# Kernel tuning notes

Measured on AMD Instinct MI355X. Metric: run time of the kernel, lower is better.

Reference implementation:

```python
import jax, jax.numpy as jnp
import numpy as np

B, T, N, D_OBJ = 8, 32, 10, 2048
N_VERB, N_OBJCLS = 157, 353
D_EMB, D_VERB = 512, 2048


def setup_inputs() -> dict:
    key = jax.random.key(0)
    k1, k2, k3, k4, k5 = jax.random.split(key, 5)
    objects_features = jax.random.normal(k1, (B, T, N, D_OBJ), dtype=jnp.float32)
    fm_context = jax.random.normal(k2, (B, T, D_VERB), dtype=jnp.float32)
    obj_id = jax.random.randint(k3, (B, T, N, N_OBJCLS), 0, 2, dtype=jnp.int32)
    W = jax.random.normal(k4, (D_OBJ, D_EMB), dtype=jnp.float32) * 0.02
    b = jnp.zeros((D_EMB,), dtype=jnp.float32)
    A_o2v = jnp.full((N_VERB, N_OBJCLS), 1.0 / N_VERB, dtype=jnp.float32)
    return {"objects_features": objects_features, "fm_context": fm_context,
            "obj_id": obj_id, "W": W, "b": b, "A_o2v": A_o2v}


def reference(objects_features, fm_context, obj_id, W, b, A_o2v):
    D = obj_id.shape[-1]
    # one-hot cleanup: all-zero row -> class 0; multi-hot row -> last nonzero class
    row_sum = obj_id.sum(-1)                                  # (B,T,N)
    last_nz = (D - 1) - jnp.argmax(jnp.flip(obj_id, -1), -1)  # last nonzero index
    cls = jnp.where(row_sum == 0, 0, last_nz)                 # (B,T,N)

    obj_embedded = objects_features @ W + b                   # (B,T,N,D_emb)

    # subA[b,t,n,v] = A_o2v[v, cls[b,t,n]]
    subA = A_o2v.T[cls]                                       # (B,T,N,V)

    afforded = jnp.einsum('btnv,btnd->btvd', subA, obj_embedded)  # (B,T,V,D_emb)

    V = A_o2v.shape[0]
    ctx = jnp.broadcast_to(fm_context[:, :, None, :],
                           (afforded.shape[0], afforded.shape[1], V, fm_context.shape[-1]))
    vo_actions = jnp.concatenate([afforded, ctx], axis=-1)    # (B,T,V,D_emb+D_verb)
    return vo_actions.mean(axis=1)                            # (B,V,D_emb+D_verb)
```

## Files before the change

kernel.cpp:

```cpp
#include <hip/hip_runtime.h>


typedef __attribute__((ext_vector_type(8))) short short8;
typedef __attribute__((ext_vector_type(8))) unsigned short us8;
typedef __attribute__((ext_vector_type(4))) unsigned short us4;
typedef __attribute__((ext_vector_type(4))) float f32x4;

#define OFF_CTX  0
#define OFF_SAT  65536
#define OFF_WT   1048576
#define OFF_PART 3145728

static __device__ inline unsigned short f2bf(float x) {
    unsigned int u = __builtin_bit_cast(unsigned int, x);
    u += 0x7fffu + ((u >> 16) & 1u);
    return (unsigned short)(u >> 16);
}
static __device__ inline void gl16(const void* g, void* l) {
    __builtin_amdgcn_global_load_lds(
        (__attribute__((address_space(1))) void*)(g),
        (__attribute__((address_space(3))) void*)(l), 16, 0, 0);
}

__global__ __launch_bounds__(256) void k_prep(
    const float* __restrict__ W, const float* __restrict__ fm,
    const int* __restrict__ obj, const float* __restrict__ A,
    unsigned short* __restrict__ Wt, float* __restrict__ ctx,
    unsigned short* __restrict__ sAT)
{
    __shared__ float t[32][33];
    __shared__ int lcls[64];
    int bx = blockIdx.x, tid = threadIdx.x;

    if (bx < 1024) {
        int r0 = (bx >> 4) * 32, c0 = (bx & 15) * 32;
        int rr = tid >> 3, cc = (tid & 7) * 4;
        float4 v = *(const float4*)&W[(size_t)(r0 + rr) * 512 + c0 + cc];
        t[rr][cc] = v.x; t[rr][cc+1] = v.y; t[rr][cc+2] = v.z; t[rr][cc+3] = v.w;
        __syncthreads();
        us4 o = { f2bf(t[cc][rr]), f2bf(t[cc+1][rr]), f2bf(t[cc+2][rr]), f2bf(t[cc+3][rr]) };
        *(us4*)&Wt[(size_t)(c0 + rr) * 2048 + r0 + cc] = o;
    } else if (bx < 1088) {
        int id = (bx - 1024) * 256 + tid;
        int b = id >> 11, d = id & 2047;
        const float* p = fm + (size_t)b * 32 * 2048 + d;
        float s = 0.f;
        #pragma unroll
        for (int tt = 0; tt < 32; tt++) s += p[(size_t)tt * 2048];
        ctx[id] = s * (1.0f / 32.0f);
    } else {
        int blk = bx - 1088;
        int b = blk / 5, i0 = (blk % 5) * 64;
        int w = tid >> 6, lane = tid & 63;
        for (int rr = 0; rr < 16; rr++) {
            int il = w * 16 + rr;
            const int* p = obj + ((size_t)b * 320 + i0 + il) * 353;
            int last = -1;
            #pragma unroll
            for (int base = 0; base < 384; base += 64) {
                int idx = base + lane;
                int v = (idx < 353) ? p[idx] : 0;
                unsigned long long m = __ballot(v != 0);
                if (m) last = base + 63 - __clzll(m);
            }
            if (lane == 0) lcls[il] = (last < 0) ? 0 : last;
        }
        __syncthreads();
        #pragma unroll
        for (int q = 0; q < 6; q++) {
            int u = q * 256 + tid;
            int v = u >> 3, i8 = u & 7;
            us8 o = {};
            if (v < 157) {
                #pragma unroll
                for (int j = 0; j < 8; j++)
                    o[j] = f2bf(A[v * 353 + lcls[i8 * 8 + j]] * (1.0f / 32.0f));
            }
            *(us8*)&sAT[((size_t)b * 192 + v) * 320 + i0 + i8 * 8] = o;
        }
    }
}

__global__ __launch_bounds__(256) void k_gemmE(
    const float* __restrict__ feat, const unsigned short* __restrict__ Wt,
    float* __restrict__ part)
{
    int bx = blockIdx.x;
    int ks = bx & 3, nt = (bx >> 2) & 3, mt = bx >> 4;
    int m0 = mt * 64, n0 = nt * 128, k0 = ks * 512;
    int b = m0 / 320, i0 = m0 % 320;

    __shared__ __align__(16) unsigned short la[2][64 * 64];
    __shared__ __align__(16) unsigned short lb[2][128 * 64];

    int tid = threadIdx.x, lane = tid & 63, w = tid >> 6;
    int wm = (w >> 1) * 32, wn = (w & 1) * 64;
    int fr = lane & 15, fk = lane >> 4;

    int ar = tid >> 2, acol = (tid & 3) * 16;
    const float* gA = feat + (size_t)(m0 + ar) * 2048 + k0 + acol;
    int asl0 = ((tid & 3) * 2 + 0) ^ (ar & 7);
    int asl1 = ((tid & 3) * 2 + 1) ^ (ar & 7);

    const unsigned short* gB[4];
    #pragma unroll
    for (int c = 0; c < 4; c++) {
        int s = c * 256 + tid, er = s >> 3, ch = s & 7;
        gB[c] = Wt + (size_t)(n0 + er) * 2048 + k0 + ((ch ^ (er & 7)) << 3);
    }

    f32x4 acc[2][4] = {};
    f32x4 a4[4];

    auto loadA = [&](int kk) {
        #pragma unroll
        for (int j = 0; j < 4; j++) a4[j] = *(const f32x4*)(gA + kk + j * 4);
    };
    auto stageB = [&](int buf, int kk) {
        #pragma unroll
        for (int c = 0; c < 4; c++)
            gl16(gB[c] + kk, &lb[buf][(c * 256 + tid) * 8]);
    };
    auto writeA = [&](int buf) {
        us8 o0, o1;
        #pragma unroll
        for (int j = 0; j < 4; j++) { o0[j] = f2bf(a4[0][j]); o0[j+4] = f2bf(a4[1][j]); }
        #pragma unroll
        for (int j = 0; j < 4; j++) { o1[j] = f2bf(a4[2][j]); o1[j+4] = f2bf(a4[3][j]); }
        *(us8*)&la[buf][ar * 64 + (asl0 << 3)] = o0;
        *(us8*)&la[buf][ar * 64 + (asl1 << 3)] = o1;
    };
    auto compute = [&](int buf) {
        #pragma unroll
        for (int k2 = 0; k2 < 2; k2++) {
            short8 af[2], bf[4];
            #pragma unroll
            for (int mi = 0; mi < 2; mi++) {
                int r = wm + mi * 16 + fr;
                af[mi] = *(const short8*)&la[buf][r * 64 + (((k2 * 4 + fk) ^ (r & 7)) << 3)];
            }
            #pragma unroll
            for (int ni = 0; ni < 4; ni++) {
                int r = wn + ni * 16 + fr;
                bf[ni] = *(const short8*)&lb[buf][r * 64 + (((k2 * 4 + fk) ^ (r & 7)) << 3)];
            }
            #pragma unroll
            for (int mi = 0; mi < 2; mi++)
                #pragma unroll
                for (int ni = 0; ni < 4; ni++)
                    acc[mi][ni] = __builtin_amdgcn_mfma_f32_16x16x32_bf16(
                        af[mi], bf[ni], acc[mi][ni], 0, 0, 0);
        }
    };

    loadA(0); stageB(0, 0); writeA(0);
    __syncthreads();
    int cur = 0;
    #pragma unroll 1
    for (int t = 0; t < 8; t++) {
        if (t < 7) { loadA((t + 1) * 64); stageB(cur ^ 1, (t + 1) * 64); }
        compute(cur);
        if (t < 7) writeA(cur ^ 1);
        __syncthreads();
        cur ^= 1;
    }

    #pragma unroll
    for (int mi = 0; mi < 2; mi++) {
        int i = i0 + wm + mi * 16 + fk * 4;
        #pragma unroll
        for (int ni = 0; ni < 4; ni++) {
            int e = n0 + wn + ni * 16 + fr;
            *(f32x4*)&part[((size_t)(b * 512 + e) * 4 + ks) * 320 + i] = acc[mi][ni];
        }
    }
}

__global__ __launch_bounds__(256) void k_out(
    const unsigned short* __restrict__ sAT, const float* __restrict__ part,
    const float* __restrict__ bias, const float* __restrict__ ctx,
    float* __restrict__ out)
{
    if (blockIdx.x >= 96) {
        int id = (blockIdx.x - 96) * 256 + threadIdx.x;
        int q = id & 511, bv = id >> 9, b = bv / 157;
        float4 v = *(const float4*)&ctx[((size_t)b << 11) + q * 4];
        *(float4*)&out[(size_t)bv * 2560 + 512 + q * 4] = v;
        return;
    }
    int bx = blockIdx.x;
    int b = bx / 12, r = bx % 12;
    int v0 = (r >> 2) * 64, e0 = (r & 3) * 128;

    __shared__ __align__(16) unsigned short la[2][64 * 32];
    __shared__ __align__(16) unsigned short lb[2][128 * 32];

    int tid = threadIdx.x, lane = tid & 63, w = tid >> 6;
    int wm = (w >> 1) * 32, wn = (w & 1) * 64;
    int fr = lane & 15, fk = lane >> 4;

    int aer = tid >> 2, ach = tid & 3;
    const unsigned short* gA = sAT + ((size_t)b * 192 + v0 + aer) * 320
                                   + ((ach ^ (aer & 3)) << 3);
    const float* pb = part + (size_t)b * 512 * 4 * 320;

    f32x4 acc[2][4] = {};
    f32x4 s0, s1, s2, s3;
    float be0, be1, be2, be3;

    auto loadB = [&](int kk) {
        f32x4* sp[4] = { &s0, &s1, &s2, &s3 };
        float* bp[4] = { &be0, &be1, &be2, &be3 };
        #pragma unroll
        for (int q = 0; q < 4; q++) {
            int u = q * 256 + tid, e = u >> 3, i4 = u & 7;
            const float* base = pb + (size_t)(e0 + e) * 4 * 320 + kk + i4 * 4;
            f32x4 s = *(const f32x4*)(base);
            s += *(const f32x4*)(base + 320);
            s += *(const f32x4*)(base + 640);
            s += *(const f32x4*)(base + 960);
            *sp[q] = s;
            *bp[q] = bias[e0 + e];
        }
    };
    auto writeB = [&](int buf) {
        f32x4 sv[4] = { s0, s1, s2, s3 };
        float bv[4] = { be0, be1, be2, be3 };
        #pragma unroll
        for (int q = 0; q < 4; q++) {
            int u = q * 256 + tid, e = u >> 3, i4 = u & 7;
            f32x4 s = sv[q];
            float be = bv[q];
            us4 o = { f2bf(s[0] + be), f2bf(s[1] + be), f2bf(s[2] + be), f2bf(s[3] + be) };
            *(us4*)&lb[buf][e * 32 + ((((i4 >> 1) ^ (e & 3)) << 3) + (i4 & 1) * 4)] = o;
        }
    };
    auto compute = [&](int buf) {
        short8 af[2], bf[4];
        #pragma unroll
        for (int mi = 0; mi < 2; mi++) {
            int rr = wm + mi * 16 + fr;
            af[mi] = *(const short8*)&la[buf][rr * 32 + ((fk ^ (rr & 3)) << 3)];
        }
        #pragma unroll
        for (int ni = 0; ni < 4; ni++) {
            int rr = wn + ni * 16 + fr;
            bf[ni] = *(const short8*)&lb[buf][rr * 32 + ((fk ^ (rr & 3)) << 3)];
        }
        #pragma unroll
        for (int mi = 0; mi < 2; mi++)
            #pragma unroll
            for (int ni = 0; ni < 4; ni++)
                acc[mi][ni] = __builtin_amdgcn_mfma_f32_16x16x32_bf16(
                    af[mi], bf[ni], acc[mi][ni], 0, 0, 0);
    };

    gl16(gA, &la[0][tid * 8]);
    loadB(0); writeB(0);
    __syncthreads();
    int cur = 0;
    #pragma unroll 1
    for (int t = 0; t < 10; t++) {
        if (t < 9) { gl16(gA + (t + 1) * 32, &la[cur ^ 1][tid * 8]); loadB((t + 1) * 32); }
        compute(cur);
        if (t < 9) writeB(cur ^ 1);
        __syncthreads();
        cur ^= 1;
    }

    #pragma unroll
    for (int mi = 0; mi < 2; mi++) {
        int vb = v0 + wm + mi * 16 + fk * 4;
        #pragma unroll
        for (int ni = 0; ni < 4; ni++) {
            int e = e0 + wn + ni * 16 + fr;
            #pragma unroll
            for (int rr = 0; rr < 4; rr++) {
                int v = vb + rr;
                if (v < 157)
                    out[((size_t)b * 157 + v) * 2560 + e] = acc[mi][ni][rr];
            }
        }
    }
}

extern "C" void kernel_launch(void* const* d_in, const int* in_sizes, int n_in,
                              void* d_out, int out_size, void* d_ws, size_t ws_size,
                              hipStream_t stream)
{
    const float* feat = (const float*)d_in[0];
    const float* fm   = (const float*)d_in[1];
    const int*   obj  = (const int*)d_in[2];
    const float* W    = (const float*)d_in[3];
    const float* bias = (const float*)d_in[4];
    const float* A    = (const float*)d_in[5];
    float* out = (float*)d_out;

    char* ws = (char*)d_ws;
    float*          ctx  = (float*)(ws + OFF_CTX);
    unsigned short* sAT  = (unsigned short*)(ws + OFF_SAT);
    unsigned short* Wt   = (unsigned short*)(ws + OFF_WT);
    float*          part = (float*)(ws + OFF_PART);

    k_prep <<<1128, 256, 0, stream>>>(W, fm, obj, A, Wt, ctx, sAT);
    k_gemmE<<<640, 256, 0, stream>>>(feat, Wt, part);
    k_out  <<<2608, 256, 0, stream>>>(sAT, part, bias, ctx, out);
}
```

Measured before the change: 128.9 us.

## Pre-convert features to bf16 and split class extraction into own kernel

Adds a pass in k_prep that converts the fp32 object features to bf16 in workspace, so the GEMM can stage both A and B tiles straight into LDS with global_load_lds instead of loading fp32 into registers and converting. The one-hot class decoding moves into a separate k_cls kernel with one wavefront per row, rather than serial loops inside the sAT blocks. The aim is to cut register pressure and latency in the GEMM main loop. In exchange the features are read in fp32 and written and reread in bf16 (about 10 MB extra traffic), and there is one more kernel launch.

```diff
diff --git a/kernel.cpp b/kernel.cpp
--- a/kernel.cpp
+++ b/kernel.cpp
@@ -9,7 +9,9 @@
 #define OFF_CTX  0
 #define OFF_SAT  65536
 #define OFF_WT   1048576
-#define OFF_PART 3145728
+#define OFF_FB   3145728
+#define OFF_PART 13631488
+#define OFF_CLS  39845888
 
 static __device__ inline unsigned short f2bf(float x) {
     unsigned int u = __builtin_bit_cast(unsigned int, x);
@@ -22,26 +24,55 @@
         (__attribute__((address_space(3))) void*)(l), 16, 0, 0);
 }
 
+__global__ void k_cls(const int* __restrict__ obj_id, int* __restrict__ cls)
+{
+    int row  = blockIdx.x * 4 + (threadIdx.x >> 6);
+    int lane = threadIdx.x & 63;
+    if (row >= 2560) return;
+    const int* p = obj_id + (size_t)row * 353;
+    int last = -1;
+    #pragma unroll
+    for (int base = 0; base < 384; base += 64) {
+        int idx = base + lane;
+        int v = (idx < 353) ? p[idx] : 0;
+        unsigned long long m = __ballot(v != 0);
+        if (m) last = base + 63 - __clzll(m);
+    }
+    if (lane == 0) cls[row] = (last < 0) ? 0 : last;
+}
+
 __global__ __launch_bounds__(256) void k_prep(
     const float* __restrict__ W, const float* __restrict__ fm,
-    const int* __restrict__ obj, const float* __restrict__ A,
+    const float* __restrict__ feat, const int* __restrict__ cls,
+    const float* __restrict__ A,
     unsigned short* __restrict__ Wt, float* __restrict__ ctx,
-    unsigned short* __restrict__ sAT)
+    unsigned short* __restrict__ featb, unsigned short* __restrict__ sAT)
 {
     __shared__ float t[32][33];
     __shared__ int lcls[64];
     int bx = blockIdx.x, tid = threadIdx.x;
 
-    if (bx < 1024) {
-        int r0 = (bx >> 4) * 32, c0 = (bx & 15) * 32;
+    if (bx < 1280) {
+        size_t id = (size_t)bx * 256 + tid;
+        const float* p = feat + id * 16;
+        us8 o0, o1;
+        #pragma unroll
+        for (int j = 0; j < 8; j++) o0[j] = f2bf(p[j]);
+        #pragma unroll
+        for (int j = 0; j < 8; j++) o1[j] = f2bf(p[8 + j]);
+        *(us8*)&featb[id * 16] = o0;
+        *(us8*)&featb[id * 16 + 8] = o1;
+    } else if (bx < 2304) {
+        int b2 = bx - 1280;
+        int r0 = (b2 >> 4) * 32, c0 = (b2 & 15) * 32;
         int rr = tid >> 3, cc = (tid & 7) * 4;
         float4 v = *(const float4*)&W[(size_t)(r0 + rr) * 512 + c0 + cc];
         t[rr][cc] = v.x; t[rr][cc+1] = v.y; t[rr][cc+2] = v.z; t[rr][cc+3] = v.w;
         __syncthreads();
         us4 o = { f2bf(t[cc][rr]), f2bf(t[cc+1][rr]), f2bf(t[cc+2][rr]), f2bf(t[cc+3][rr]) };
         *(us4*)&Wt[(size_t)(c0 + rr) * 2048 + r0 + cc] = o;
-    } else if (bx < 1088) {
-        int id = (bx - 1024) * 256 + tid;
+    } else if (bx < 2368) {
+        int id = (bx - 2304) * 256 + tid;
         int b = id >> 11, d = id & 2047;
         const float* p = fm + (size_t)b * 32 * 2048 + d;
         float s = 0.f;
@@ -49,22 +80,9 @@
         for (int tt = 0; tt < 32; tt++) s += p[(size_t)tt * 2048];
         ctx[id] = s * (1.0f / 32.0f);
     } else {
-        int blk = bx - 1088;
+        int blk = bx - 2368;
         int b = blk / 5, i0 = (blk % 5) * 64;
-        int w = tid >> 6, lane = tid & 63;
-        for (int rr = 0; rr < 16; rr++) {
-            int il = w * 16 + rr;
-            const int* p = obj + ((size_t)b * 320 + i0 + il) * 353;
-            int last = -1;
-            #pragma unroll
-            for (int base = 0; base < 384; base += 64) {
-                int idx = base + lane;
-                int v = (idx < 353) ? p[idx] : 0;
-                unsigned long long m = __ballot(v != 0);
-                if (m) last = base + 63 - __clzll(m);
-            }
-            if (lane == 0) lcls[il] = (last < 0) ? 0 : last;
-        }
+        if (tid < 64) lcls[tid] = cls[b * 320 + i0 + tid];
         __syncthreads();
         #pragma unroll
         for (int q = 0; q < 6; q++) {
@@ -82,7 +100,7 @@
 }
 
 __global__ __launch_bounds__(256) void k_gemmE(
-    const float* __restrict__ feat, const unsigned short* __restrict__ Wt,
+    const unsigned short* __restrict__ featb, const unsigned short* __restrict__ Wt,
     float* __restrict__ part)
 {
     int bx = blockIdx.x;
@@ -97,11 +115,12 @@
     int wm = (w >> 1) * 32, wn = (w & 1) * 64;
     int fr = lane & 15, fk = lane >> 4;
 
-    int ar = tid >> 2, acol = (tid & 3) * 16;
-    const float* gA = feat + (size_t)(m0 + ar) * 2048 + k0 + acol;
-    int asl0 = ((tid & 3) * 2 + 0) ^ (ar & 7);
-    int asl1 = ((tid & 3) * 2 + 1) ^ (ar & 7);
-
+    const unsigned short* gA[2];
+    #pragma unroll
+    for (int c = 0; c < 2; c++) {
+        int s = c * 256 + tid, ar = s >> 3, ch = s & 7;
+        gA[c] = featb + (size_t)(b * 320 + i0 + ar) * 2048 + k0 + ((ch ^ (ar & 7)) << 3);
+    }
     const unsigned short* gB[4];
     #pragma unroll
     for (int c = 0; c < 4; c++) {
@@ -110,25 +129,12 @@
     }
 
     f32x4 acc[2][4] = {};
-    f32x4 a4[4];
-
-    auto loadA = [&](int kk) {
-        #pragma unroll
-        for (int j = 0; j < 4; j++) a4[j] = *(const f32x4*)(gA + kk + j * 4);
-    };
-    auto stageB = [&](int buf, int kk) {
-        #pragma unroll
-        for (int c = 0; c < 4; c++)
-            gl16(gB[c] + kk, &lb[buf][(c * 256 + tid) * 8]);
-    };
-    auto writeA = [&](int buf) {
-        us8 o0, o1;
-        #pragma unroll
-        for (int j = 0; j < 4; j++) { o0[j] = f2bf(a4[0][j]); o0[j+4] = f2bf(a4[1][j]); }
-        #pragma unroll
-        for (int j = 0; j < 4; j++) { o1[j] = f2bf(a4[2][j]); o1[j+4] = f2bf(a4[3][j]); }
-        *(us8*)&la[buf][ar * 64 + (asl0 << 3)] = o0;
-        *(us8*)&la[buf][ar * 64 + (asl1 << 3)] = o1;
+
+    auto stage = [&](int buf, int kk) {
+        #pragma unroll
+        for (int c = 0; c < 2; c++) gl16(gA[c] + kk, &la[buf][(c * 256 + tid) * 8]);
+        #pragma unroll
+        for (int c = 0; c < 4; c++) gl16(gB[c] + kk, &lb[buf][(c * 256 + tid) * 8]);
     };
     auto compute = [&](int buf) {
         #pragma unroll
@@ -153,14 +159,13 @@
         }
     };
 
-    loadA(0); stageB(0, 0); writeA(0);
+    stage(0, 0);
     __syncthreads();
     int cur = 0;
     #pragma unroll 1
     for (int t = 0; t < 8; t++) {
-        if (t < 7) { loadA((t + 1) * 64); stageB(cur ^ 1, (t + 1) * 64); }
+        if (t < 7) stage(cur ^ 1, (t + 1) * 64);
         compute(cur);
-        if (t < 7) writeA(cur ^ 1);
         __syncthreads();
         cur ^= 1;
     }
@@ -297,12 +302,15 @@
     float* out = (float*)d_out;
 
     char* ws = (char*)d_ws;
-    float*          ctx  = (float*)(ws + OFF_CTX);
-    unsigned short* sAT  = (unsigned short*)(ws + OFF_SAT);
-    unsigned short* Wt   = (unsigned short*)(ws + OFF_WT);
-    float*          part = (float*)(ws + OFF_PART);
-
-    k_prep <<<1128, 256, 0, stream>>>(W, fm, obj, A, Wt, ctx, sAT);
-    k_gemmE<<<640, 256, 0, stream>>>(feat, Wt, part);
+    float*          ctx   = (float*)(ws + OFF_CTX);
+    unsigned short* sAT   = (unsigned short*)(ws + OFF_SAT);
+    unsigned short* Wt    = (unsigned short*)(ws + OFF_WT);
+    unsigned short* featb = (unsigned short*)(ws + OFF_FB);
+    float*          part  = (float*)(ws + OFF_PART);
+    int*            cls   = (int*)(ws + OFF_CLS);
+
+    k_cls  <<<640, 256, 0, stream>>>(obj, cls);
+    k_prep <<<2408, 256, 0, stream>>>(W, fm, feat, cls, A, Wt, ctx, featb, sAT);
+    k_gemmE<<<640, 256, 0, stream>>>(featb, Wt, part);
     k_out  <<<2608, 256, 0, stream>>>(sAT, part, bias, ctx, out);
 }
```

Result: faster. 118.0 us (-8.4%).
